# Optimization experiments

Measured on AMD Instinct MI355X. Metric: run time of the kernel, lower is better.

## Reference

```python
import jax, jax.numpy as jnp
import numpy as np
from jax import lax

N, CI, CO, H, W = 2, 256, 256, 64, 64
K, G, DIL, PAD, STRIDE = 3, 8, 1, 1, 1
P = K * K
CG = CO // G  # group channels = 32


def setup_inputs() -> dict:
    key = jax.random.key(0)
    ks = jax.random.split(key, 24)
    r = lambda i, shape, s=1.0: jax.random.normal(ks[i], shape, jnp.float32) * s
    u = lambda i, shape: jax.random.uniform(ks[i], shape, jnp.float32, 0.5, 1.5)
    return dict(
        x=r(0, (N, CI, H, W)),
        conv1_w=r(1, (CO, CI), CI ** -0.5),
        bn1_g=u(2, (CO,)), bn1_b=r(3, (CO,), 0.1), bn1_m=r(4, (CO,), 0.1), bn1_v=u(5, (CO,)),
        inproj_w=r(6, (CO, CO), CO ** -0.5), inproj_b=r(7, (CO,), 0.02),
        dw_w=r(8, (CO, 1, K, K), 0.2), dw_b=r(9, (CO,), 0.02),
        ln_g=u(10, (CO,)), ln_b=r(11, (CO,), 0.02),
        off_w=r(12, (CO, G * P * 2), CO ** -0.5), off_b=jnp.zeros((G * P * 2,), jnp.float32),
        mask_w=r(13, (CO, G * P), CO ** -0.5), mask_b=jnp.zeros((G * P,), jnp.float32),
        outproj_w=r(14, (CO, CO), CO ** -0.5), outproj_b=r(15, (CO,), 0.02),
        bn2_g=u(16, (CO,)), bn2_b=r(17, (CO,), 0.1), bn2_m=r(18, (CO,), 0.1), bn2_v=u(19, (CO,)),
    )


def _bn(x, g, b, m, v, eps):
    # inference-mode BatchNorm2d on NCHW
    return (x - m[:, None, None]) * (g[:, None, None] * lax.rsqrt(v[:, None, None] + eps)) + b[:, None, None]


def _dcn_core(t, offset, mask):
    # t: (N,H,W,C) projected input; offset: (N,H,W,G*P*2); mask: (N,H,W,G,P) softmaxed
    xp = jnp.pad(t, ((0, 0), (PAD, PAD), (PAD, PAD), (0, 0)))
    H_, W_ = H + 2 * PAD, W + 2 * PAD
    # reference points (sample centers), normalized to padded size
    ry = ((DIL * (K - 1)) / 2 + 0.5 + STRIDE * jnp.arange(H, dtype=t.dtype)) / H_
    rx = ((DIL * (K - 1)) / 2 + 0.5 + STRIDE * jnp.arange(W, dtype=t.dtype)) / W_
    base = (DIL * (K - 1)) // 2
    gx = jnp.linspace(-base, -base + (K - 1) * DIL, K, dtype=t.dtype) / W_
    gy = jnp.linspace(-base, -base + (K - 1) * DIL, K, dtype=t.dtype) / H_
    gxx, gyy = jnp.meshgrid(gx, gy, indexing='ij')  # x varies along axis 0 (torch meshgrid order)
    grid = jnp.stack([gxx, gyy], -1).reshape(P, 2)  # (P,2)
    off = offset.reshape(N, H, W, G, P, 2) / jnp.array([W_, H_], t.dtype)
    loc_x = rx[None, None, :, None, None] + grid[:, 0][None, None, None, None] + off[..., 0]  # (N,H,W,G,P)
    loc_y = ry[None, :, None, None, None] + grid[:, 1][None, None, None, None] + off[..., 1]
    # grid_sample(align_corners=False): pixel = norm*size - 0.5
    px = jnp.transpose(loc_x * W_ - 0.5, (0, 3, 1, 2, 4)).reshape(N, G, H * W * P)
    py = jnp.transpose(loc_y * H_ - 0.5, (0, 3, 1, 2, 4)).reshape(N, G, H * W * P)
    # grouped channels-last image: (N,G,H_*W_,CG)
    xg = jnp.transpose(xp.reshape(N, H_, W_, G, CG), (0, 3, 1, 2, 4)).reshape(N, G, H_ * W_, CG)
    x0 = jnp.floor(px)
    y0 = jnp.floor(py)
    wx1 = px - x0
    wy1 = py - y0
    x0i = x0.astype(jnp.int32)
    y0i = y0.astype(jnp.int32)

    def corner(xi, yi, w):
        valid = (xi >= 0) & (xi <= W_ - 1) & (yi >= 0) & (yi <= H_ - 1)
        idx = jnp.clip(yi, 0, H_ - 1) * W_ + jnp.clip(xi, 0, W_ - 1)
        v = jnp.take_along_axis(xg, idx[..., None], axis=2)  # (N,G,M,CG)
        return v * jnp.where(valid, w, 0.0)[..., None]

    sampled = (corner(x0i, y0i, (1 - wx1) * (1 - wy1))
               + corner(x0i + 1, y0i, wx1 * (1 - wy1))
               + corner(x0i, y0i + 1, (1 - wx1) * wy1)
               + corner(x0i + 1, y0i + 1, wx1 * wy1))
    sampled = sampled.reshape(N, G, H * W, P, CG)
    mg = jnp.transpose(mask, (0, 3, 1, 2, 4)).reshape(N, G, H * W, P)
    out = jnp.einsum('nglpc,nglp->nglc', sampled, mg)
    return jnp.transpose(out, (0, 2, 1, 3)).reshape(N, H, W, G * CG)


def reference(x, conv1_w, bn1_g, bn1_b, bn1_m, bn1_v, inproj_w, inproj_b, dw_w, dw_b,
              ln_g, ln_b, off_w, off_b, mask_w, mask_b, outproj_w, outproj_b,
              bn2_g, bn2_b, bn2_m, bn2_v):
    # Conv(inc, ouc, k=1): 1x1 conv (no bias) + BN(eps=1e-3) + SiLU
    y = jnp.einsum('nchw,oc->nohw', x, conv1_w)
    y = jax.nn.silu(_bn(y, bn1_g, bn1_b, bn1_m, bn1_v, 1e-3))
    t = jnp.transpose(y, (0, 2, 3, 1))  # NHWC
    xproj = t @ inproj_w + inproj_b     # input_proj Linear
    # offset/mask branch: depthwise conv (k=3,s=1,p=1) -> LN over C -> GELU
    z = lax.conv_general_dilated(y, dw_w, (1, 1), ((PAD, PAD), (PAD, PAD)),
                                 feature_group_count=CO,
                                 dimension_numbers=('NCHW', 'OIHW', 'NCHW')) + dw_b[None, :, None, None]
    z = jnp.transpose(z, (0, 2, 3, 1))
    mu = jnp.mean(z, -1, keepdims=True)
    var = jnp.var(z, -1, keepdims=True)
    z = (z - mu) * lax.rsqrt(var + 1e-5) * ln_g + ln_b
    z = jax.nn.gelu(z, approximate=False)
    offset = z @ off_w + off_b  # (N,H,W,G*P*2)
    mask = jax.nn.softmax((z @ mask_w + mask_b).reshape(N, H, W, G, P), axis=-1)
    s = _dcn_core(xproj, offset, mask)
    s = s @ outproj_w + outproj_b  # output_proj Linear
    o = jnp.transpose(s, (0, 3, 1, 2))  # back to NCHW
    return jax.nn.silu(_bn(o, bn2_g, bn2_b, bn2_m, bn2_v, 1e-5))
```

## Files before the change

### kernel.cpp

```cpp
#include <hip/hip_runtime.h>
#include <math.h>

#define CC    256
#define HH    64
#define WW    64
#define HWSZ  4096
#define NPIX  8192
#define MT    16
#define ASTR  264

typedef __attribute__((ext_vector_type(8))) short short8;
typedef __attribute__((ext_vector_type(4))) float f32x4;

__device__ __forceinline__ float silu_f(float x) { return x / (1.f + __expf(-x)); }

__device__ __forceinline__ short f2bf(float f) {
    unsigned u = __float_as_uint(f);
    unsigned r = (u + 0x7fffu + ((u >> 16) & 1u)) >> 16;
    return (short)r;
}
__device__ __forceinline__ unsigned pk2(float a, float b) {
    return (unsigned)(unsigned short)f2bf(a) | ((unsigned)(unsigned short)f2bf(b) << 16);
}

__global__ void k_prep(const float* __restrict__ cw, const float* __restrict__ ipw,
                       const float* __restrict__ offw, const float* __restrict__ maskw,
                       const float* __restrict__ opw,
                       const float* __restrict__ offb, const float* __restrict__ maskb,
                       const float* __restrict__ g1, const float* __restrict__ b1,
                       const float* __restrict__ m1, const float* __restrict__ v1,
                       const float* __restrict__ g2, const float* __restrict__ b2,
                       const float* __restrict__ m2, const float* __restrict__ v2,
                       short* __restrict__ Wc1b, short* __restrict__ Wipb,
                       short* __restrict__ Whb, short* __restrict__ Wopb,
                       float* __restrict__ bh, float* __restrict__ sc1, float* __restrict__ sh1,
                       float* __restrict__ sc2, float* __restrict__ sh2) {
    int o = blockIdx.x, c = threadIdx.x;
    Wc1b[o * CC + c] = f2bf(cw[o * CC + c]);
    Wipb[o * CC + c] = f2bf(ipw[c * CC + o]);
    float hv = 0.f;
    if (o < 144) hv = offw[c * 144 + o];
    else if (o < 216) hv = maskw[c * 72 + (o - 144)];
    Whb[o * CC + c] = f2bf(hv);
    Wopb[o * CC + c] = f2bf(opw[c * CC + o]);
    if (o == 0) {
        float bv = 0.f;
        if (c < 144) bv = offb[c];
        else if (c < 216) bv = maskb[c - 144];
        bh[c] = bv;
        float s1 = g1[c] * rsqrtf(v1[c] + 1e-3f);
        sc1[c] = s1; sh1[c] = b1[c] - m1[c] * s1;
        float s2 = g2[c] * rsqrtf(v2[c] + 1e-5f);
        sc2[c] = s2; sh2[c] = b2[c] - m2[c] * s2;
    }
}

__device__ __forceinline__ void stage_tile(const float* __restrict__ src, short* As, int tid) {
#pragma unroll
    for (int k = 0; k < 4; ++k) {
        int f = tid + k * 256;
        float4 v = ((const float4*)src)[f];
        int pix = f >> 6, c = (f & 63) * 4;
        *(uint2*)(As + pix * ASTR + c) = make_uint2(pk2(v.x, v.y), pk2(v.z, v.w));
    }
}

__device__ __forceinline__ void mfma_gemm(const short* As, const short* __restrict__ Wb,
                                          int lane, int n0, f32x4 acc[4]) {
    const int m = lane & 15, q = lane >> 4;
#pragma unroll
    for (int kk = 0; kk < 8; ++kk) {
        int c0 = kk * 32 + q * 8;
        short8 a = *(const short8*)(As + m * ASTR + c0);
#pragma unroll
        for (int nt = 0; nt < 4; ++nt) {
            short8 b = *(const short8*)(Wb + (size_t)(n0 + nt * 16 + m) * CC + c0);
            acc[nt] = __builtin_amdgcn_mfma_f32_16x16x32_bf16(a, b, acc[nt], 0, 0, 0);
        }
    }
}

__global__ void k_conv_in(const float* __restrict__ x, const short* __restrict__ Wc1b,
                          const short* __restrict__ Wipb, const float* __restrict__ sc1,
                          const float* __restrict__ sh1, const float* __restrict__ ipb,
                          float* __restrict__ y, float* __restrict__ xp) {
    __shared__ __align__(16) short As[MT * ASTR];
    int tid = threadIdx.x;
    int pix0 = blockIdx.x * MT;
    int n = pix0 >> 12, hw0 = pix0 & (HWSZ - 1);
    const float* xn = x + (size_t)n * CC * HWSZ;
    {
        int i4 = (tid & 3) * 4;
#pragma unroll
        for (int rep = 0; rep < 4; ++rep) {
            int c = (tid >> 2) + rep * 64;
            float4 v = *(const float4*)(xn + (size_t)c * HWSZ + hw0 + i4);
            As[(i4 + 0) * ASTR + c] = f2bf(v.x);
            As[(i4 + 1) * ASTR + c] = f2bf(v.y);
            As[(i4 + 2) * ASTR + c] = f2bf(v.z);
            As[(i4 + 3) * ASTR + c] = f2bf(v.w);
        }
    }
    __syncthreads();
    int lane = tid & 63, n0 = (tid >> 6) * 64;
    int col = lane & 15, qr = (lane >> 4) * 4;
    f32x4 acc[4];
#pragma unroll
    for (int nt = 0; nt < 4; ++nt) acc[nt] = (f32x4){0.f, 0.f, 0.f, 0.f};
    mfma_gemm(As, Wc1b, lane, n0, acc);
    __syncthreads();
#pragma unroll
    for (int nt = 0; nt < 4; ++nt) {
        int o = n0 + nt * 16 + col;
        float sc = sc1[o], sh = sh1[o];
#pragma unroll
        for (int r = 0; r < 4; ++r) {
            int pix = qr + r;
            float val = silu_f(acc[nt][r] * sc + sh);
            y[(size_t)(pix0 + pix) * CC + o] = val;
            As[pix * ASTR + o] = f2bf(val);
        }
    }
    __syncthreads();
#pragma unroll
    for (int nt = 0; nt < 4; ++nt) acc[nt] = (f32x4){0.f, 0.f, 0.f, 0.f};
    mfma_gemm(As, Wipb, lane, n0, acc);
#pragma unroll
    for (int nt = 0; nt < 4; ++nt) {
        int o = n0 + nt * 16 + col;
        float bo = ipb[o];
#pragma unroll
        for (int r = 0; r < 4; ++r)
            xp[(size_t)(pix0 + qr + r) * CC + o] = acc[nt][r] + bo;
    }
}

__global__ __launch_bounds__(256, 2) void k_dwln(
        const float* __restrict__ y, const float* __restrict__ dww,
        const float* __restrict__ dwb, const float* __restrict__ lng,
        const float* __restrict__ lnb, float* __restrict__ z) {
    int tid = threadIdx.x;
    int wv = tid >> 6, l = tid & 63;
    int pix = blockIdx.x * 4 + wv;
    int n = pix >> 12, hw = pix & (HWSZ - 1);
    int h = hw >> 6, wx_ = hw & 63;
    int c0 = l * 4;
    float wloc[36];
    const float4* wp = (const float4*)(dww + c0 * 9);
#pragma unroll
    for (int k = 0; k < 9; ++k) ((float4*)wloc)[k] = wp[k];
    float4 acc = *(const float4*)(dwb + c0);
    const float* yn = y + (size_t)n * HWSZ * CC;
#pragma unroll
    for (int ky = 0; ky < 3; ++ky) {
        int yy = h + ky - 1;
        if (yy < 0 || yy >= HH) continue;
#pragma unroll
        for (int kx = 0; kx < 3; ++kx) {
            int xx = wx_ + kx - 1;
            if (xx < 0 || xx >= WW) continue;
            float4 yv = *(const float4*)(yn + (size_t)((yy << 6) + xx) * CC + c0);
            int t = ky * 3 + kx;
            acc.x += yv.x * wloc[0 * 9 + t];
            acc.y += yv.y * wloc[1 * 9 + t];
            acc.z += yv.z * wloc[2 * 9 + t];
            acc.w += yv.w * wloc[3 * 9 + t];
        }
    }
    float s1 = acc.x + acc.y + acc.z + acc.w;
    float s2 = acc.x * acc.x + acc.y * acc.y + acc.z * acc.z + acc.w * acc.w;
#pragma unroll
    for (int off = 32; off > 0; off >>= 1) {
        s1 += __shfl_xor(s1, off);
        s2 += __shfl_xor(s2, off);
    }
    float mu = s1 * (1.f / 256.f);
    float var = s2 * (1.f / 256.f) - mu * mu;
    float rs = rsqrtf(var + 1e-5f);
    float4 gv = *(const float4*)(lng + c0);
    float4 bv = *(const float4*)(lnb + c0);
    float4 zv;
    zv.x = (acc.x - mu) * rs * gv.x + bv.x;
    zv.y = (acc.y - mu) * rs * gv.y + bv.y;
    zv.z = (acc.z - mu) * rs * gv.z + bv.z;
    zv.w = (acc.w - mu) * rs * gv.w + bv.w;
    zv.x = 0.5f * zv.x * (1.f + erff(zv.x * 0.70710678118654752f));
    zv.y = 0.5f * zv.y * (1.f + erff(zv.y * 0.70710678118654752f));
    zv.z = 0.5f * zv.z * (1.f + erff(zv.z * 0.70710678118654752f));
    zv.w = 0.5f * zv.w * (1.f + erff(zv.w * 0.70710678118654752f));
    *(float4*)(z + (size_t)pix * CC + c0) = zv;
}

__global__ void k_heads(const float* __restrict__ z, const short* __restrict__ Whb,
                        const float* __restrict__ bh, float* __restrict__ offs,
                        float* __restrict__ msk) {
    __shared__ __align__(16) short As[MT * ASTR];
    __shared__ float ml[MT * 76];
    int tid = threadIdx.x;
    int pix0 = blockIdx.x * MT;
    stage_tile(z + (size_t)pix0 * CC, As, tid);
    __syncthreads();
    int lane = tid & 63, n0 = (tid >> 6) * 64;
    int col = lane & 15, qr = (lane >> 4) * 4;
    f32x4 acc[4];
#pragma unroll
    for (int nt = 0; nt < 4; ++nt) acc[nt] = (f32x4){0.f, 0.f, 0.f, 0.f};
    mfma_gemm(As, Whb, lane, n0, acc);
#pragma unroll
    for (int nt = 0; nt < 4; ++nt) {
        int o = n0 + nt * 16 + col;
        float bo = bh[o];
#pragma unroll
        for (int r = 0; r < 4; ++r) {
            int pix = qr + r;
            float v = acc[nt][r] + bo;
            if (o < 144) offs[(size_t)(pix0 + pix) * 144 + o] = v;
            else if (o < 216) ml[pix * 76 + (o - 144)] = v;
        }
    }
    __syncthreads();
    if (tid < 128) {
        int pi = tid >> 3, g = tid & 7;
        const float* row = ml + pi * 76 + g * 9;
        float mx = -1e30f;
#pragma unroll
        for (int p = 0; p < 9; ++p) mx = fmaxf(mx, row[p]);
        float e[9], s = 0.f;
#pragma unroll
        for (int p = 0; p < 9; ++p) { e[p] = __expf(row[p] - mx); s += e[p]; }
        float inv = 1.f / s;
        float* mp = msk + (size_t)(pix0 + pi) * 72 + g * 9;
#pragma unroll
        for (int p = 0; p < 9; ++p) mp[p] = e[p] * inv;
    }
}

__global__ __launch_bounds__(256, 2) void k_dcn(
        const float* __restrict__ xp, const float* __restrict__ offs,
        const float* __restrict__ msk, float* __restrict__ sout) {
    __shared__ float loff[4][144];
    __shared__ float lm[4][72];
    int tid = threadIdx.x;
    int wv = tid >> 6, l = tid & 63;
    int pix = blockIdx.x * 4 + wv;
    const float* op = offs + (size_t)pix * 144;
    const float* mp = msk + (size_t)pix * 72;
    loff[wv][l] = op[l];
    loff[wv][64 + l] = op[64 + l];
    if (l < 16) loff[wv][128 + l] = op[128 + l];
    lm[wv][l] = mp[l];
    if (l < 8) lm[wv][64 + l] = mp[64 + l];
    __syncthreads();
    int n = pix >> 12, hw = pix & (HWSZ - 1);
    int h = hw >> 6, w = hw & 63;
    int g = l >> 3, q = l & 7;
    int c0 = g * 32 + q * 4;
    const float* xpn = xp + (size_t)n * HWSZ * CC;
    float4 acc = make_float4(0.f, 0.f, 0.f, 0.f);
#pragma unroll
    for (int p = 0; p < 9; ++p) {
        float ox = loff[wv][(g * 9 + p) * 2];
        float oy = loff[wv][(g * 9 + p) * 2 + 1];
        float px = (float)(w + p / 3) + ox;
        float py = (float)(h + p % 3) + oy;
        float fx = floorf(px), fy = floorf(py);
        float wx1 = px - fx, wy1 = py - fy;
        int x0 = (int)fx, y0 = (int)fy;
        int x1 = x0 + 1, y1 = y0 + 1;
        float mval = lm[wv][g * 9 + p];
        float w00 = (1.f - wx1) * (1.f - wy1) * mval;
        float w10 = wx1 * (1.f - wy1) * mval;
        float w01 = (1.f - wx1) * wy1 * mval;
        float w11 = wx1 * wy1 * mval;
        if (x0 >= 1 && x0 <= WW && y0 >= 1 && y0 <= HH) {
            float4 s = *(const float4*)(xpn + (size_t)(((y0 - 1) << 6) + (x0 - 1)) * CC + c0);
            acc.x += w00 * s.x; acc.y += w00 * s.y; acc.z += w00 * s.z; acc.w += w00 * s.w;
        }
        if (x1 >= 1 && x1 <= WW && y0 >= 1 && y0 <= HH) {
            float4 s = *(const float4*)(xpn + (size_t)(((y0 - 1) << 6) + (x1 - 1)) * CC + c0);
            acc.x += w10 * s.x; acc.y += w10 * s.y; acc.z += w10 * s.z; acc.w += w10 * s.w;
        }
        if (x0 >= 1 && x0 <= WW && y1 >= 1 && y1 <= HH) {
            float4 s = *(const float4*)(xpn + (size_t)(((y1 - 1) << 6) + (x0 - 1)) * CC + c0);
            acc.x += w01 * s.x; acc.y += w01 * s.y; acc.z += w01 * s.z; acc.w += w01 * s.w;
        }
        if (x1 >= 1 && x1 <= WW && y1 >= 1 && y1 <= HH) {
            float4 s = *(const float4*)(xpn + (size_t)(((y1 - 1) << 6) + (x1 - 1)) * CC + c0);
            acc.x += w11 * s.x; acc.y += w11 * s.y; acc.z += w11 * s.z; acc.w += w11 * s.w;
        }
    }
    *(float4*)(sout + (size_t)pix * CC + c0) = acc;
}

__global__ void k_out(const float* __restrict__ s, const short* __restrict__ Wopb,
                      const float* __restrict__ opb, const float* __restrict__ sc2,
                      const float* __restrict__ sh2, float* __restrict__ out) {
    __shared__ __align__(16) short As[MT * ASTR];
    __shared__ float xs[MT * 260];
    int tid = threadIdx.x;
    int pix0 = blockIdx.x * MT;
    stage_tile(s + (size_t)pix0 * CC, As, tid);
    __syncthreads();
    int lane = tid & 63, n0 = (tid >> 6) * 64;
    int col = lane & 15, qr = (lane >> 4) * 4;
    f32x4 acc[4];
#pragma unroll
    for (int nt = 0; nt < 4; ++nt) acc[nt] = (f32x4){0.f, 0.f, 0.f, 0.f};
    mfma_gemm(As, Wopb, lane, n0, acc);
#pragma unroll
    for (int nt = 0; nt < 4; ++nt) {
        int o = n0 + nt * 16 + col;
        float bo = opb[o], sc = sc2[o], sh = sh2[o];
#pragma unroll
        for (int r = 0; r < 4; ++r)
            xs[(qr + r) * 260 + o] = silu_f((acc[nt][r] + bo) * sc + sh);
    }
    __syncthreads();
    int n = pix0 >> 12, hw0 = pix0 & (HWSZ - 1);
    float* on = out + (size_t)n * CC * HWSZ + (size_t)tid * HWSZ + hw0;
#pragma unroll
    for (int i4 = 0; i4 < MT; i4 += 4) {
        float4 ov;
        ov.x = xs[(i4 + 0) * 260 + tid];
        ov.y = xs[(i4 + 1) * 260 + tid];
        ov.z = xs[(i4 + 2) * 260 + tid];
        ov.w = xs[(i4 + 3) * 260 + tid];
        *(float4*)(on + i4) = ov;
    }
}

extern "C" void kernel_launch(void* const* d_in, const int* in_sizes, int n_in,
                              void* d_out, int out_size, void* d_ws, size_t ws_size,
                              hipStream_t stream) {
    const float* x        = (const float*)d_in[0];
    const float* conv1_w  = (const float*)d_in[1];
    const float* bn1_g    = (const float*)d_in[2];
    const float* bn1_b    = (const float*)d_in[3];
    const float* bn1_m    = (const float*)d_in[4];
    const float* bn1_v    = (const float*)d_in[5];
    const float* inproj_w = (const float*)d_in[6];
    const float* inproj_b = (const float*)d_in[7];
    const float* dw_w     = (const float*)d_in[8];
    const float* dw_b     = (const float*)d_in[9];
    const float* ln_g     = (const float*)d_in[10];
    const float* ln_b     = (const float*)d_in[11];
    const float* off_w    = (const float*)d_in[12];
    const float* off_b    = (const float*)d_in[13];
    const float* mask_w   = (const float*)d_in[14];
    const float* mask_b   = (const float*)d_in[15];
    const float* outproj_w = (const float*)d_in[16];
    const float* outproj_b = (const float*)d_in[17];
    const float* bn2_g    = (const float*)d_in[18];
    const float* bn2_b    = (const float*)d_in[19];
    const float* bn2_m    = (const float*)d_in[20];
    const float* bn2_v    = (const float*)d_in[21];
    float* out = (float*)d_out;

    short* Wc1b = (short*)d_ws;
    short* Wipb = Wc1b + 65536;
    short* Whb  = Wipb + 65536;
    short* Wopb = Whb + 65536;
    float* fp   = (float*)(Wopb + 65536);
    float* bh   = fp;
    float* sc1  = bh + 256;
    float* sh1  = sc1 + 256;
    float* sc2  = sh1 + 256;
    float* sh2  = sc2 + 256;
    float* y    = sh2 + 256;
    float* xp   = y + 2097152;
    float* z    = xp + 2097152;
    float* offs = z + 2097152;
    float* msk  = offs + 1179648;
    float* sbuf = z;

    k_prep<<<dim3(CC), dim3(CC), 0, stream>>>(conv1_w, inproj_w, off_w, mask_w, outproj_w,
                                              off_b, mask_b, bn1_g, bn1_b, bn1_m, bn1_v,
                                              bn2_g, bn2_b, bn2_m, bn2_v,
                                              Wc1b, Wipb, Whb, Wopb, bh, sc1, sh1, sc2, sh2);
    k_conv_in<<<dim3(NPIX / MT), dim3(256), 0, stream>>>(x, Wc1b, Wipb, sc1, sh1, inproj_b, y, xp);
    k_dwln<<<dim3(NPIX / 4), dim3(256), 0, stream>>>(y, dw_w, dw_b, ln_g, ln_b, z);
    k_heads<<<dim3(NPIX / MT), dim3(256), 0, stream>>>(z, Whb, bh, offs, msk);
    k_dcn<<<dim3(NPIX / 4), dim3(256), 0, stream>>>(xp, offs, msk, sbuf);
    k_out<<<dim3(NPIX / MT), dim3(256), 0, stream>>>(sbuf, Wopb, outproj_b, sc2, sh2, out);
}
```

Before: 177.8 us.

## Fuse depthwise-LN, offset/mask heads, deformable sampling and output proj into one kernel

```diff
diff --git a/kernel.cpp b/kernel.cpp
--- a/kernel.cpp
+++ b/kernel.cpp
@@ -55,16 +55,6 @@
     }
 }
 
-__device__ __forceinline__ void stage_tile(const float* __restrict__ src, short* As, int tid) {
-#pragma unroll
-    for (int k = 0; k < 4; ++k) {
-        int f = tid + k * 256;
-        float4 v = ((const float4*)src)[f];
-        int pix = f >> 6, c = (f & 63) * 4;
-        *(uint2*)(As + pix * ASTR + c) = make_uint2(pk2(v.x, v.y), pk2(v.z, v.w));
-    }
-}
-
 __device__ __forceinline__ void mfma_gemm(const short* As, const short* __restrict__ Wb,
                                           int lane, int n0, f32x4 acc[4]) {
     const int m = lane & 15, q = lane >> 4;
@@ -135,90 +125,103 @@
     }
 }
 
-__global__ __launch_bounds__(256, 2) void k_dwln(
-        const float* __restrict__ y, const float* __restrict__ dww,
-        const float* __restrict__ dwb, const float* __restrict__ lng,
-        const float* __restrict__ lnb, float* __restrict__ z) {
+__global__ void k_tail(const float* __restrict__ y, const float* __restrict__ xp,
+                       const float* __restrict__ dww, const float* __restrict__ dwb,
+                       const float* __restrict__ lng, const float* __restrict__ lnb,
+                       const short* __restrict__ Whb, const float* __restrict__ bh,
+                       const short* __restrict__ Wopb, const float* __restrict__ opb,
+                       const float* __restrict__ sc2, const float* __restrict__ sh2,
+                       float* __restrict__ out) {
+    __shared__ __align__(16) short As[MT * ASTR];
+    __shared__ __align__(16) float buf[4672];
+    float* ml   = buf;
+    float* loff = buf + 1216;
+    float* lm   = buf + 3520;
+    float* xs   = buf;
+
     int tid = threadIdx.x;
-    int wv = tid >> 6, l = tid & 63;
-    int pix = blockIdx.x * 4 + wv;
-    int n = pix >> 12, hw = pix & (HWSZ - 1);
-    int h = hw >> 6, wx_ = hw & 63;
-    int c0 = l * 4;
-    float wloc[36];
-    const float4* wp = (const float4*)(dww + c0 * 9);
-#pragma unroll
-    for (int k = 0; k < 9; ++k) ((float4*)wloc)[k] = wp[k];
-    float4 acc = *(const float4*)(dwb + c0);
-    const float* yn = y + (size_t)n * HWSZ * CC;
-#pragma unroll
-    for (int ky = 0; ky < 3; ++ky) {
-        int yy = h + ky - 1;
-        if (yy < 0 || yy >= HH) continue;
-#pragma unroll
-        for (int kx = 0; kx < 3; ++kx) {
-            int xx = wx_ + kx - 1;
-            if (xx < 0 || xx >= WW) continue;
-            float4 yv = *(const float4*)(yn + (size_t)((yy << 6) + xx) * CC + c0);
-            int t = ky * 3 + kx;
-            acc.x += yv.x * wloc[0 * 9 + t];
-            acc.y += yv.y * wloc[1 * 9 + t];
-            acc.z += yv.z * wloc[2 * 9 + t];
-            acc.w += yv.w * wloc[3 * 9 + t];
-        }
-    }
-    float s1 = acc.x + acc.y + acc.z + acc.w;
-    float s2 = acc.x * acc.x + acc.y * acc.y + acc.z * acc.z + acc.w * acc.w;
-#pragma unroll
-    for (int off = 32; off > 0; off >>= 1) {
-        s1 += __shfl_xor(s1, off);
-        s2 += __shfl_xor(s2, off);
-    }
-    float mu = s1 * (1.f / 256.f);
-    float var = s2 * (1.f / 256.f) - mu * mu;
-    float rs = rsqrtf(var + 1e-5f);
-    float4 gv = *(const float4*)(lng + c0);
-    float4 bv = *(const float4*)(lnb + c0);
-    float4 zv;
-    zv.x = (acc.x - mu) * rs * gv.x + bv.x;
-    zv.y = (acc.y - mu) * rs * gv.y + bv.y;
-    zv.z = (acc.z - mu) * rs * gv.z + bv.z;
-    zv.w = (acc.w - mu) * rs * gv.w + bv.w;
-    zv.x = 0.5f * zv.x * (1.f + erff(zv.x * 0.70710678118654752f));
-    zv.y = 0.5f * zv.y * (1.f + erff(zv.y * 0.70710678118654752f));
-    zv.z = 0.5f * zv.z * (1.f + erff(zv.z * 0.70710678118654752f));
-    zv.w = 0.5f * zv.w * (1.f + erff(zv.w * 0.70710678118654752f));
-    *(float4*)(z + (size_t)pix * CC + c0) = zv;
-}
-
-__global__ void k_heads(const float* __restrict__ z, const short* __restrict__ Whb,
-                        const float* __restrict__ bh, float* __restrict__ offs,
-                        float* __restrict__ msk) {
-    __shared__ __align__(16) short As[MT * ASTR];
-    __shared__ float ml[MT * 76];
-    int tid = threadIdx.x;
+    int lane = tid & 63, wv = tid >> 6;
     int pix0 = blockIdx.x * MT;
-    stage_tile(z + (size_t)pix0 * CC, As, tid);
-    __syncthreads();
-    int lane = tid & 63, n0 = (tid >> 6) * 64;
+    int n = pix0 >> 12, hw0 = pix0 & (HWSZ - 1);
+    int h = hw0 >> 6, w0 = hw0 & 63;
+    int c0 = lane * 4;
+
+    {
+        float wloc[36];
+        const float4* wp4 = (const float4*)(dww + c0 * 9);
+#pragma unroll
+        for (int k = 0; k < 9; ++k) ((float4*)wloc)[k] = wp4[k];
+        float4 dwbv = *(const float4*)(dwb + c0);
+        float4 lngv = *(const float4*)(lng + c0);
+        float4 lnbv = *(const float4*)(lnb + c0);
+        const float* yn = y + (size_t)n * HWSZ * CC;
+#pragma unroll
+        for (int i = 0; i < 4; ++i) {
+            int pix = wv * 4 + i;
+            int w = w0 + pix;
+            float4 acc = dwbv;
+#pragma unroll
+            for (int ky = 0; ky < 3; ++ky) {
+                int yy = h + ky - 1;
+                if (yy < 0 || yy >= HH) continue;
+#pragma unroll
+                for (int kx = 0; kx < 3; ++kx) {
+                    int xx = w + kx - 1;
+                    if (xx < 0 || xx >= WW) continue;
+                    float4 yv = *(const float4*)(yn + (size_t)((yy << 6) + xx) * CC + c0);
+                    int t = ky * 3 + kx;
+                    acc.x += yv.x * wloc[0 * 9 + t];
+                    acc.y += yv.y * wloc[1 * 9 + t];
+                    acc.z += yv.z * wloc[2 * 9 + t];
+                    acc.w += yv.w * wloc[3 * 9 + t];
+                }
+            }
+            float s1 = acc.x + acc.y + acc.z + acc.w;
+            float s2 = acc.x * acc.x + acc.y * acc.y + acc.z * acc.z + acc.w * acc.w;
+#pragma unroll
+            for (int off = 32; off > 0; off >>= 1) {
+                s1 += __shfl_xor(s1, off);
+                s2 += __shfl_xor(s2, off);
+            }
+            float mu = s1 * (1.f / 256.f);
+            float var = s2 * (1.f / 256.f) - mu * mu;
+            float rs = rsqrtf(var + 1e-5f);
+            float4 zv;
+            zv.x = (acc.x - mu) * rs * lngv.x + lnbv.x;
+            zv.y = (acc.y - mu) * rs * lngv.y + lnbv.y;
+            zv.z = (acc.z - mu) * rs * lngv.z + lnbv.z;
+            zv.w = (acc.w - mu) * rs * lngv.w + lnbv.w;
+            zv.x = 0.5f * zv.x * (1.f + erff(zv.x * 0.70710678118654752f));
+            zv.y = 0.5f * zv.y * (1.f + erff(zv.y * 0.70710678118654752f));
+            zv.z = 0.5f * zv.z * (1.f + erff(zv.z * 0.70710678118654752f));
+            zv.w = 0.5f * zv.w * (1.f + erff(zv.w * 0.70710678118654752f));
+            *(uint2*)(As + pix * ASTR + c0) = make_uint2(pk2(zv.x, zv.y), pk2(zv.z, zv.w));
+        }
+    }
+    __syncthreads();
+
+    int n0 = wv * 64;
     int col = lane & 15, qr = (lane >> 4) * 4;
-    f32x4 acc[4];
-#pragma unroll
-    for (int nt = 0; nt < 4; ++nt) acc[nt] = (f32x4){0.f, 0.f, 0.f, 0.f};
-    mfma_gemm(As, Whb, lane, n0, acc);
-#pragma unroll
-    for (int nt = 0; nt < 4; ++nt) {
-        int o = n0 + nt * 16 + col;
-        float bo = bh[o];
-#pragma unroll
-        for (int r = 0; r < 4; ++r) {
-            int pix = qr + r;
-            float v = acc[nt][r] + bo;
-            if (o < 144) offs[(size_t)(pix0 + pix) * 144 + o] = v;
-            else if (o < 216) ml[pix * 76 + (o - 144)] = v;
-        }
-    }
-    __syncthreads();
+    {
+        f32x4 acc[4];
+#pragma unroll
+        for (int nt = 0; nt < 4; ++nt) acc[nt] = (f32x4){0.f, 0.f, 0.f, 0.f};
+        mfma_gemm(As, Whb, lane, n0, acc);
+#pragma unroll
+        for (int nt = 0; nt < 4; ++nt) {
+            int o = n0 + nt * 16 + col;
+            float bo = bh[o];
+#pragma unroll
+            for (int r = 0; r < 4; ++r) {
+                float v = acc[nt][r] + bo;
+                int pix = qr + r;
+                if (o < 144) loff[pix * 144 + o] = v;
+                else if (o < 216) ml[pix * 76 + (o - 144)] = v;
+            }
+        }
+    }
+    __syncthreads();
+
     if (tid < 128) {
         int pi = tid >> 3, g = tid & 7;
         const float* row = ml + pi * 76 + g * 9;
@@ -229,94 +232,72 @@
 #pragma unroll
         for (int p = 0; p < 9; ++p) { e[p] = __expf(row[p] - mx); s += e[p]; }
         float inv = 1.f / s;
-        float* mp = msk + (size_t)(pix0 + pi) * 72 + g * 9;
+        float* mp = lm + pi * 72 + g * 9;
 #pragma unroll
         for (int p = 0; p < 9; ++p) mp[p] = e[p] * inv;
     }
-}
-
-__global__ __launch_bounds__(256, 2) void k_dcn(
-        const float* __restrict__ xp, const float* __restrict__ offs,
-        const float* __restrict__ msk, float* __restrict__ sout) {
-    __shared__ float loff[4][144];
-    __shared__ float lm[4][72];
-    int tid = threadIdx.x;
-    int wv = tid >> 6, l = tid & 63;
-    int pix = blockIdx.x * 4 + wv;
-    const float* op = offs + (size_t)pix * 144;
-    const float* mp = msk + (size_t)pix * 72;
-    loff[wv][l] = op[l];
-    loff[wv][64 + l] = op[64 + l];
-    if (l < 16) loff[wv][128 + l] = op[128 + l];
-    lm[wv][l] = mp[l];
-    if (l < 8) lm[wv][64 + l] = mp[64 + l];
-    __syncthreads();
-    int n = pix >> 12, hw = pix & (HWSZ - 1);
-    int h = hw >> 6, w = hw & 63;
-    int g = l >> 3, q = l & 7;
-    int c0 = g * 32 + q * 4;
-    const float* xpn = xp + (size_t)n * HWSZ * CC;
-    float4 acc = make_float4(0.f, 0.f, 0.f, 0.f);
-#pragma unroll
-    for (int p = 0; p < 9; ++p) {
-        float ox = loff[wv][(g * 9 + p) * 2];
-        float oy = loff[wv][(g * 9 + p) * 2 + 1];
-        float px = (float)(w + p / 3) + ox;
-        float py = (float)(h + p % 3) + oy;
-        float fx = floorf(px), fy = floorf(py);
-        float wx1 = px - fx, wy1 = py - fy;
-        int x0 = (int)fx, y0 = (int)fy;
-        int x1 = x0 + 1, y1 = y0 + 1;
-        float mval = lm[wv][g * 9 + p];
-        float w00 = (1.f - wx1) * (1.f - wy1) * mval;
-        float w10 = wx1 * (1.f - wy1) * mval;
-        float w01 = (1.f - wx1) * wy1 * mval;
-        float w11 = wx1 * wy1 * mval;
-        if (x0 >= 1 && x0 <= WW && y0 >= 1 && y0 <= HH) {
-            float4 s = *(const float4*)(xpn + (size_t)(((y0 - 1) << 6) + (x0 - 1)) * CC + c0);
-            acc.x += w00 * s.x; acc.y += w00 * s.y; acc.z += w00 * s.z; acc.w += w00 * s.w;
-        }
-        if (x1 >= 1 && x1 <= WW && y0 >= 1 && y0 <= HH) {
-            float4 s = *(const float4*)(xpn + (size_t)(((y0 - 1) << 6) + (x1 - 1)) * CC + c0);
-            acc.x += w10 * s.x; acc.y += w10 * s.y; acc.z += w10 * s.z; acc.w += w10 * s.w;
-        }
-        if (x0 >= 1 && x0 <= WW && y1 >= 1 && y1 <= HH) {
-            float4 s = *(const float4*)(xpn + (size_t)(((y1 - 1) << 6) + (x0 - 1)) * CC + c0);
-            acc.x += w01 * s.x; acc.y += w01 * s.y; acc.z += w01 * s.z; acc.w += w01 * s.w;
-        }
-        if (x1 >= 1 && x1 <= WW && y1 >= 1 && y1 <= HH) {
-            float4 s = *(const float4*)(xpn + (size_t)(((y1 - 1) << 6) + (x1 - 1)) * CC + c0);
-            acc.x += w11 * s.x; acc.y += w11 * s.y; acc.z += w11 * s.z; acc.w += w11 * s.w;
-        }
-    }
-    *(float4*)(sout + (size_t)pix * CC + c0) = acc;
-}
-
-__global__ void k_out(const float* __restrict__ s, const short* __restrict__ Wopb,
-                      const float* __restrict__ opb, const float* __restrict__ sc2,
-                      const float* __restrict__ sh2, float* __restrict__ out) {
-    __shared__ __align__(16) short As[MT * ASTR];
-    __shared__ float xs[MT * 260];
-    int tid = threadIdx.x;
-    int pix0 = blockIdx.x * MT;
-    stage_tile(s + (size_t)pix0 * CC, As, tid);
-    __syncthreads();
-    int lane = tid & 63, n0 = (tid >> 6) * 64;
-    int col = lane & 15, qr = (lane >> 4) * 4;
-    f32x4 acc[4];
-#pragma unroll
-    for (int nt = 0; nt < 4; ++nt) acc[nt] = (f32x4){0.f, 0.f, 0.f, 0.f};
-    mfma_gemm(As, Wopb, lane, n0, acc);
-#pragma unroll
-    for (int nt = 0; nt < 4; ++nt) {
-        int o = n0 + nt * 16 + col;
-        float bo = opb[o], sc = sc2[o], sh = sh2[o];
-#pragma unroll
-        for (int r = 0; r < 4; ++r)
-            xs[(qr + r) * 260 + o] = silu_f((acc[nt][r] + bo) * sc + sh);
-    }
-    __syncthreads();
-    int n = pix0 >> 12, hw0 = pix0 & (HWSZ - 1);
+    __syncthreads();
+
+    {
+        int g = lane >> 3;
+        const float* xpn = xp + (size_t)n * HWSZ * CC;
+#pragma unroll
+        for (int i = 0; i < 4; ++i) {
+            int pix = wv * 4 + i;
+            int w = w0 + pix;
+            float4 acc = make_float4(0.f, 0.f, 0.f, 0.f);
+#pragma unroll
+            for (int p = 0; p < 9; ++p) {
+                float ox = loff[pix * 144 + (g * 9 + p) * 2];
+                float oy = loff[pix * 144 + (g * 9 + p) * 2 + 1];
+                float px = (float)(w + p / 3) + ox;
+                float py = (float)(h + p % 3) + oy;
+                float fx = floorf(px), fy = floorf(py);
+                float wx1 = px - fx, wy1 = py - fy;
+                int x0 = (int)fx, y0 = (int)fy;
+                int x1 = x0 + 1, y1 = y0 + 1;
+                float mval = lm[pix * 72 + g * 9 + p];
+                float w00 = (1.f - wx1) * (1.f - wy1) * mval;
+                float w10 = wx1 * (1.f - wy1) * mval;
+                float w01 = (1.f - wx1) * wy1 * mval;
+                float w11 = wx1 * wy1 * mval;
+                if (x0 >= 1 && x0 <= WW && y0 >= 1 && y0 <= HH) {
+                    float4 s = *(const float4*)(xpn + (size_t)(((y0 - 1) << 6) + (x0 - 1)) * CC + c0);
+                    acc.x += w00 * s.x; acc.y += w00 * s.y; acc.z += w00 * s.z; acc.w += w00 * s.w;
+                }
+                if (x1 >= 1 && x1 <= WW && y0 >= 1 && y0 <= HH) {
+                    float4 s = *(const float4*)(xpn + (size_t)(((y0 - 1) << 6) + (x1 - 1)) * CC + c0);
+                    acc.x += w10 * s.x; acc.y += w10 * s.y; acc.z += w10 * s.z; acc.w += w10 * s.w;
+                }
+                if (x0 >= 1 && x0 <= WW && y1 >= 1 && y1 <= HH) {
+                    float4 s = *(const float4*)(xpn + (size_t)(((y1 - 1) << 6) + (x0 - 1)) * CC + c0);
+                    acc.x += w01 * s.x; acc.y += w01 * s.y; acc.z += w01 * s.z; acc.w += w01 * s.w;
+                }
+                if (x1 >= 1 && x1 <= WW && y1 >= 1 && y1 <= HH) {
+                    float4 s = *(const float4*)(xpn + (size_t)(((y1 - 1) << 6) + (x1 - 1)) * CC + c0);
+                    acc.x += w11 * s.x; acc.y += w11 * s.y; acc.z += w11 * s.z; acc.w += w11 * s.w;
+                }
+            }
+            *(uint2*)(As + pix * ASTR + c0) = make_uint2(pk2(acc.x, acc.y), pk2(acc.z, acc.w));
+        }
+    }
+    __syncthreads();
+
+    {
+        f32x4 acc[4];
+#pragma unroll
+        for (int nt = 0; nt < 4; ++nt) acc[nt] = (f32x4){0.f, 0.f, 0.f, 0.f};
+        mfma_gemm(As, Wopb, lane, n0, acc);
+#pragma unroll
+        for (int nt = 0; nt < 4; ++nt) {
+            int o = n0 + nt * 16 + col;
+            float bo = opb[o], sc = sc2[o], sh = sh2[o];
+#pragma unroll
+            for (int r = 0; r < 4; ++r)
+                xs[(qr + r) * 260 + o] = silu_f((acc[nt][r] + bo) * sc + sh);
+        }
+    }
+    __syncthreads();
     float* on = out + (size_t)n * CC * HWSZ + (size_t)tid * HWSZ + hw0;
 #pragma unroll
     for (int i4 = 0; i4 < MT; i4 += 4) {
@@ -368,18 +349,12 @@
     float* sh2  = sc2 + 256;
     float* y    = sh2 + 256;
     float* xp   = y + 2097152;
-    float* z    = xp + 2097152;
-    float* offs = z + 2097152;
-    float* msk  = offs + 1179648;
-    float* sbuf = z;
 
     k_prep<<<dim3(CC), dim3(CC), 0, stream>>>(conv1_w, inproj_w, off_w, mask_w, outproj_w,
                                               off_b, mask_b, bn1_g, bn1_b, bn1_m, bn1_v,
                                               bn2_g, bn2_b, bn2_m, bn2_v,
                                               Wc1b, Wipb, Whb, Wopb, bh, sc1, sh1, sc2, sh2);
     k_conv_in<<<dim3(NPIX / MT), dim3(256), 0, stream>>>(x, Wc1b, Wipb, sc1, sh1, inproj_b, y, xp);
-    k_dwln<<<dim3(NPIX / 4), dim3(256), 0, stream>>>(y, dw_w, dw_b, ln_g, ln_b, z);
-    k_heads<<<dim3(NPIX / MT), dim3(256), 0, stream>>>(z, Whb, bh, offs, msk);
-    k_dcn<<<dim3(NPIX / 4), dim3(256), 0, stream>>>(xp, offs, msk, sbuf);
-    k_out<<<dim3(NPIX / MT), dim3(256), 0, stream>>>(sbuf, Wopb, outproj_b, sc2, sh2, out);
-}
+    k_tail<<<dim3(NPIX / MT), dim3(256), 0, stream>>>(y, xp, dw_w, dw_b, ln_g, ln_b,
+                                                      Whb, bh, Wopb, outproj_b, sc2, sh2, out);
+}
```

Result: slower. 190.5 us (+7.2%).
